# Performance work log

Measured on AMD Instinct MI355X. Metric: run time of the kernel, lower is better.

Reference implementation:

```python
import jax, jax.numpy as jnp
import numpy as np

N_SYS = 512      # number of crystal systems in the batch
N_ATOM = 32      # atoms per system (uniform for the reference)
N = N_SYS * N_ATOM            # 16384 total atoms
M = N_SYS * N_ATOM * N_ATOM   # 524288 dense intra-system edges
R = 16           # lattice translation points per edge
E = 128          # embed_dim
H = 8            # num_heads


def setup_inputs() -> dict:
    key = jax.random.key(0)
    ks = jax.random.split(key, 6)
    x = jax.random.normal(ks[0], (N, E), jnp.float32)
    in_proj_weight = jax.random.normal(ks[1], (3 * E, E), jnp.float32) / np.float32(np.sqrt(E))
    in_proj_bias = jnp.zeros((3 * E,), jnp.float32)
    out_proj_weight = jax.random.normal(ks[2], (E, E), jnp.float32) / np.float32(np.sqrt(E))
    out_proj_bias = jnp.zeros((E,), jnp.float32)
    # per-node per-head Gaussian exponents; must be negative for convergent lattice sums
    alpha = -(jax.random.uniform(ks[3], (N, H), jnp.float32) * 0.9 + 0.1)
    # squared distances from atom i to lattice images of atom j, up to ~5 Angstrom
    dist2 = jax.random.uniform(ks[4], (M, R), jnp.float32) * 25.0
    # dense intra-system edge list in (query-major) block order, as Crystalformer assumes
    base = (np.arange(N_SYS, dtype=np.int32) * N_ATOM)[:, None, None]
    qi = np.arange(N_ATOM, dtype=np.int32)[None, :, None]
    kj = np.arange(N_ATOM, dtype=np.int32)[None, None, :]
    e0 = np.broadcast_to(base + qi, (N_SYS, N_ATOM, N_ATOM)).reshape(-1)
    e1 = np.broadcast_to(base + kj, (N_SYS, N_ATOM, N_ATOM)).reshape(-1)
    edges = jnp.asarray(np.stack([e0, e1]), jnp.int32)
    batch = jnp.asarray(np.repeat(np.arange(N_SYS, dtype=np.int32), N_ATOM))
    return {
        "x": x,
        "in_proj_weight": in_proj_weight,
        "in_proj_bias": in_proj_bias,
        "out_proj_weight": out_proj_weight,
        "out_proj_bias": out_proj_bias,
        "alpha": alpha,
        "dist2": dist2,
        "edges": edges,
        "batch": batch,
    }


def reference(x, in_proj_weight, in_proj_bias, out_proj_weight, out_proj_bias,
              alpha, dist2, edges, batch):
    n, e = x.shape
    h = alpha.shape[1]
    dh = e // h
    # in-projection (self-attention: q = k = v = x)
    qkv = x @ in_proj_weight.T + in_proj_bias           # [N, 3E]
    q, k, v = jnp.split(qkv, 3, axis=-1)
    q = q.reshape(n, h, dh) / jnp.sqrt(jnp.asarray(dh, x.dtype))
    k = k.reshape(n, h, dh)
    v = v.reshape(n, h, dh)
    e0, e1 = edges[0], edges[1]
    # per-edge dot-product score, gathered q/k  -> [M, H]
    attn = jnp.einsum("mhd,mhd->mh", q[e0], k[e1])
    # real-domain lattice-sum attention bias: logsumexp_r(alpha_i * |r|^2)  -> [M, H]
    aw = jax.nn.logsumexp(alpha[e0][:, :, None] * dist2[:, None, :], axis=-1)
    s = attn + aw
    # segment softmax over each query's neighborhood (norm_func_mode=0 'default')
    smax = jax.ops.segment_max(s, e0, num_segments=n)   # [N, H]
    p = jnp.exp(s - smax[e0])
    denom = jax.ops.segment_sum(p, e0, num_segments=n)  # [N, H]
    p = p / denom[e0]
    # scatter-add aggregation of gathered values  -> [N, H, dh]
    out = jax.ops.segment_sum(p[:, :, None] * v[e1], e0, num_segments=n)
    # out-projection
    out = out.reshape(n, e) @ out_proj_weight.T + out_proj_bias
    return out
```

## Files before the change

### kernel.cpp

```cpp
#include <hip/hip_runtime.h>
#include <hip/hip_bf16.h>

#define LOG2E_F 1.4426950408889634f

typedef __attribute__((ext_vector_type(8))) short short8;
typedef __attribute__((ext_vector_type(4))) float f32x4;

__device__ inline unsigned short f2b(float f) {
    __hip_bfloat16 h = __float2bfloat16(f);
    return *reinterpret_cast<unsigned short*>(&h);
}

__device__ inline short8 load_frag_f32(const float* p) {
    const float4 lo = *(const float4*)p;
    const float4 hi = *(const float4*)(p + 4);
    short8 r;
    r[0] = (short)f2b(lo.x); r[1] = (short)f2b(lo.y);
    r[2] = (short)f2b(lo.z); r[3] = (short)f2b(lo.w);
    r[4] = (short)f2b(hi.x); r[5] = (short)f2b(hi.y);
    r[6] = (short)f2b(hi.z); r[7] = (short)f2b(hi.w);
    return r;
}

__global__ __launch_bounds__(512, 4) void fused_attn_kernel(
    const float* __restrict__ x, const float* __restrict__ Win,
    const float* __restrict__ bin, const float* __restrict__ Wout,
    const float* __restrict__ bout, const float* __restrict__ alpha,
    const float* __restrict__ dist2, float* __restrict__ out)
{
    __shared__ float qkvl[3][32][164];
    __shared__ unsigned short aggb[32][136];

    const int sys  = blockIdx.x;
    const int tid  = threadIdx.x;
    const int lane = tid & 63;
    const int wv   = tid >> 6;
    const int r16  = lane & 15;
    const int kg   = lane >> 4;
    const int base = sys << 5;

    short8 af[2][4];
    #pragma unroll
    for (int rt = 0; rt < 2; ++rt)
        #pragma unroll
        for (int ks = 0; ks < 4; ++ks)
            af[rt][ks] = load_frag_f32(
                x + (size_t)(base + rt * 16 + r16) * 128 + ks * 32 + kg * 8);

    #pragma unroll
    for (int j = 0; j < 3; ++j) {
        const int ct = wv * 3 + j;
        const int c  = ct * 16 + r16;
        short8 bf[4];
        #pragma unroll
        for (int ks = 0; ks < 4; ++ks)
            bf[ks] = load_frag_f32(Win + (size_t)c * 128 + ks * 32 + kg * 8);
        const float bias_v = bin[c];
        const int   bufi   = ct >> 3;
        const int   hh     = ct & 7;
        const float scale  = (bufi == 0) ? 0.25f : 1.0f;

        #pragma unroll
        for (int rt = 0; rt < 2; ++rt) {
            f32x4 acc = {0.f, 0.f, 0.f, 0.f};
            #pragma unroll
            for (int ks = 0; ks < 4; ++ks)
                acc = __builtin_amdgcn_mfma_f32_16x16x32_bf16(af[rt][ks], bf[ks], acc, 0, 0, 0);
            #pragma unroll
            for (int r = 0; r < 4; ++r) {
                const int atom = rt * 16 + kg * 4 + r;
                qkvl[bufi][atom][hh * 20 + r16] = (acc[r] + bias_v) * scale;
            }
        }
    }

    const int t     = tid & 255;
    const int khalf = tid >> 8;
    const int qi    = t >> 3;
    const int h     = t & 7;
    const float al2 = alpha[(size_t)(base + qi) * 8 + h] * LOG2E_F;

    __syncthreads();

    float qreg[16];
    {
        const float* qrow = &qkvl[0][qi][h * 20];
        #pragma unroll
        for (int d4 = 0; d4 < 4; ++d4) {
            const float4 tq = *(const float4*)(qrow + (d4 << 2));
            qreg[d4 * 4 + 0] = tq.x; qreg[d4 * 4 + 1] = tq.y;
            qreg[d4 * 4 + 2] = tq.z; qreg[d4 * 4 + 3] = tq.w;
        }
    }

    float m = -1e30f;
    float den = 0.f;
    float acc[16] = {};
    const float* dp = dist2 + ((size_t)(sys * 1024 + qi * 32) + khalf * 16) * 16;

    #pragma unroll
    for (int kk = 0; kk < 16; ++kk, dp += 16) {
        const int kj = khalf * 16 + kk;
        const float4 t0 = *(const float4*)(dp + 0);
        const float4 t1 = *(const float4*)(dp + 4);
        const float4 t2 = *(const float4*)(dp + 8);
        const float4 t3 = *(const float4*)(dp + 12);
        const float mn = fminf(
            fminf(fminf(fminf(t0.x, t0.y), fminf(t0.z, t0.w)),
                  fminf(fminf(t1.x, t1.y), fminf(t1.z, t1.w))),
            fminf(fminf(fminf(t2.x, t2.y), fminf(t2.z, t2.w)),
                  fminf(fminf(t3.x, t3.y), fminf(t3.z, t3.w))));
        const float c0 = al2 * mn;
        float e0 = __builtin_amdgcn_exp2f(fmaf(al2, t0.x, -c0));
        e0 += __builtin_amdgcn_exp2f(fmaf(al2, t0.y, -c0));
        e0 += __builtin_amdgcn_exp2f(fmaf(al2, t0.z, -c0));
        e0 += __builtin_amdgcn_exp2f(fmaf(al2, t0.w, -c0));
        float e1 = __builtin_amdgcn_exp2f(fmaf(al2, t1.x, -c0));
        e1 += __builtin_amdgcn_exp2f(fmaf(al2, t1.y, -c0));
        e1 += __builtin_amdgcn_exp2f(fmaf(al2, t1.z, -c0));
        e1 += __builtin_amdgcn_exp2f(fmaf(al2, t1.w, -c0));
        float e2 = __builtin_amdgcn_exp2f(fmaf(al2, t2.x, -c0));
        e2 += __builtin_amdgcn_exp2f(fmaf(al2, t2.y, -c0));
        e2 += __builtin_amdgcn_exp2f(fmaf(al2, t2.z, -c0));
        e2 += __builtin_amdgcn_exp2f(fmaf(al2, t2.w, -c0));
        float e3 = __builtin_amdgcn_exp2f(fmaf(al2, t3.x, -c0));
        e3 += __builtin_amdgcn_exp2f(fmaf(al2, t3.y, -c0));
        e3 += __builtin_amdgcn_exp2f(fmaf(al2, t3.z, -c0));
        e3 += __builtin_amdgcn_exp2f(fmaf(al2, t3.w, -c0));
        const float ssum = (e0 + e1) + (e2 + e3);

        const float* kr = &qkvl[1][kj][h * 20];
        const float4 k0 = *(const float4*)(kr + 0);
        const float4 k1 = *(const float4*)(kr + 4);
        const float4 k2 = *(const float4*)(kr + 8);
        const float4 k3 = *(const float4*)(kr + 12);
        float p0 = qreg[0] * k0.x, p1 = qreg[1] * k0.y;
        float p2 = qreg[2] * k0.z, p3 = qreg[3] * k0.w;
        p0 = fmaf(qreg[4],  k1.x, p0); p1 = fmaf(qreg[5],  k1.y, p1);
        p2 = fmaf(qreg[6],  k1.z, p2); p3 = fmaf(qreg[7],  k1.w, p3);
        p0 = fmaf(qreg[8],  k2.x, p0); p1 = fmaf(qreg[9],  k2.y, p1);
        p2 = fmaf(qreg[10], k2.z, p2); p3 = fmaf(qreg[11], k2.w, p3);
        p0 = fmaf(qreg[12], k3.x, p0); p1 = fmaf(qreg[13], k3.y, p1);
        p2 = fmaf(qreg[14], k3.z, p2); p3 = fmaf(qreg[15], k3.w, p3);
        const float dot = (p0 + p1) + (p2 + p3);

        const float b = fmaf(dot, LOG2E_F, c0);

        if (b - m > 8.0f) {
            const float sc = __builtin_amdgcn_exp2f(m - b);
            den *= sc;
            #pragma unroll
            for (int d = 0; d < 16; ++d) acc[d] *= sc;
            m = b;
        }
        const float p = __builtin_amdgcn_exp2f(b - m) * ssum;
        den += p;

        const float* vr = &qkvl[2][kj][h * 20];
        const float4 v0 = *(const float4*)(vr + 0);
        const float4 v1 = *(const float4*)(vr + 4);
        const float4 v2 = *(const float4*)(vr + 8);
        const float4 v3 = *(const float4*)(vr + 12);
        acc[0]  = fmaf(p, v0.x, acc[0]);  acc[1]  = fmaf(p, v0.y, acc[1]);
        acc[2]  = fmaf(p, v0.z, acc[2]);  acc[3]  = fmaf(p, v0.w, acc[3]);
        acc[4]  = fmaf(p, v1.x, acc[4]);  acc[5]  = fmaf(p, v1.y, acc[5]);
        acc[6]  = fmaf(p, v1.z, acc[6]);  acc[7]  = fmaf(p, v1.w, acc[7]);
        acc[8]  = fmaf(p, v2.x, acc[8]);  acc[9]  = fmaf(p, v2.y, acc[9]);
        acc[10] = fmaf(p, v2.z, acc[10]); acc[11] = fmaf(p, v2.w, acc[11]);
        acc[12] = fmaf(p, v3.x, acc[12]); acc[13] = fmaf(p, v3.y, acc[13]);
        acc[14] = fmaf(p, v3.z, acc[14]); acc[15] = fmaf(p, v3.w, acc[15]);
    }

    __syncthreads();
    float* exch = &qkvl[0][0][0];
    if (khalf == 1) {
        float* e = exch + t * 19;
        e[0] = m; e[1] = den;
        #pragma unroll
        for (int d = 0; d < 16; ++d) e[2 + d] = acc[d];
    }
    __syncthreads();
    if (khalf == 0) {
        const float* e = exch + t * 19;
        const float m2   = e[0];
        const float den2 = e[1];
        const float M  = fmaxf(m, m2);
        const float s1 = __builtin_amdgcn_exp2f(m - M);
        const float s2 = __builtin_amdgcn_exp2f(m2 - M);
        const float inv = 1.0f / (den * s1 + den2 * s2);
        const float a1 = s1 * inv, a2 = s2 * inv;

        unsigned short* op = &aggb[qi][h * 16];
        uint4 o0, o1;
        o0.x = (unsigned)f2b(fmaf(acc[0],  a1, e[2]  * a2)) | ((unsigned)f2b(fmaf(acc[1],  a1, e[3]  * a2)) << 16);
        o0.y = (unsigned)f2b(fmaf(acc[2],  a1, e[4]  * a2)) | ((unsigned)f2b(fmaf(acc[3],  a1, e[5]  * a2)) << 16);
        o0.z = (unsigned)f2b(fmaf(acc[4],  a1, e[6]  * a2)) | ((unsigned)f2b(fmaf(acc[5],  a1, e[7]  * a2)) << 16);
        o0.w = (unsigned)f2b(fmaf(acc[6],  a1, e[8]  * a2)) | ((unsigned)f2b(fmaf(acc[7],  a1, e[9]  * a2)) << 16);
        o1.x = (unsigned)f2b(fmaf(acc[8],  a1, e[10] * a2)) | ((unsigned)f2b(fmaf(acc[9],  a1, e[11] * a2)) << 16);
        o1.y = (unsigned)f2b(fmaf(acc[10], a1, e[12] * a2)) | ((unsigned)f2b(fmaf(acc[11], a1, e[13] * a2)) << 16);
        o1.z = (unsigned)f2b(fmaf(acc[12], a1, e[14] * a2)) | ((unsigned)f2b(fmaf(acc[13], a1, e[15] * a2)) << 16);
        o1.w = (unsigned)f2b(fmaf(acc[14], a1, e[16] * a2)) | ((unsigned)f2b(fmaf(acc[15], a1, e[17] * a2)) << 16);
        *(uint4*)op       = o0;
        *(uint4*)(op + 8) = o1;
    }

    __syncthreads();

    short8 aA[2][4];
    #pragma unroll
    for (int rt = 0; rt < 2; ++rt)
        #pragma unroll
        for (int ks = 0; ks < 4; ++ks)
            aA[rt][ks] = *(const short8*)(&aggb[rt * 16 + r16][ks * 32 + kg * 8]);

    {
        const int c = wv * 16 + r16;
        short8 bf[4];
        #pragma unroll
        for (int ks = 0; ks < 4; ++ks)
            bf[ks] = load_frag_f32(Wout + (size_t)c * 128 + ks * 32 + kg * 8);
        const float bias_v = bout[c];
        #pragma unroll
        for (int rt = 0; rt < 2; ++rt) {
            f32x4 oacc = {0.f, 0.f, 0.f, 0.f};
            #pragma unroll
            for (int ks = 0; ks < 4; ++ks)
                oacc = __builtin_amdgcn_mfma_f32_16x16x32_bf16(aA[rt][ks], bf[ks], oacc, 0, 0, 0);
            #pragma unroll
            for (int r = 0; r < 4; ++r) {
                const int row = base + rt * 16 + kg * 4 + r;
                out[(size_t)row * 128 + c] = oacc[r] + bias_v;
            }
        }
    }
}

extern "C" void kernel_launch(void* const* d_in, const int* in_sizes, int n_in,
                              void* d_out, int out_size, void* d_ws, size_t ws_size,
                              hipStream_t stream)
{
    const float* x     = (const float*)d_in[0];
    const float* Win   = (const float*)d_in[1];
    const float* bin   = (const float*)d_in[2];
    const float* Wout  = (const float*)d_in[3];
    const float* bout  = (const float*)d_in[4];
    const float* alpha = (const float*)d_in[5];
    const float* dist2 = (const float*)d_in[6];

    fused_attn_kernel<<<dim3(512), 512, 0, stream>>>(
        x, Win, bin, Wout, bout, alpha, dist2, (float*)d_out);
}
```

Baseline: 42.14 us.

## Split lattice-sum logsumexp bias into a separate precompute kernel

Adds a standalone kernel that computes log(sum_r exp2(alpha*log2e*dist2)) for every edge and head and writes it to workspace in head-major layout. The fused attention kernel then loads 16 precomputed bias values per thread instead of reading dist2 and evaluating the exponentials inline. The min-subtraction stabilisation of the exponent is dropped. The aim is to run the exponential-heavy work with more parallelism than the fused kernel allows. The cost is an extra launch and an extra 16 MB of intermediate traffic (written, then read back) on top of the existing 32 MB dist2 read.

After: 47.18 us. +12.0%, slower.

```diff
diff --git a/kernel.cpp b/kernel.cpp
--- a/kernel.cpp
+++ b/kernel.cpp
@@ -2,6 +2,7 @@
 #include <hip/hip_bf16.h>
 
 #define LOG2E_F 1.4426950408889634f
+#define M_EDGES 524288
 
 typedef __attribute__((ext_vector_type(8))) short short8;
 typedef __attribute__((ext_vector_type(4))) float f32x4;
@@ -22,11 +23,50 @@
     return r;
 }
 
+__global__ __launch_bounds__(256) void aw_kernel(
+    const float* __restrict__ alpha, const float* __restrict__ dist2,
+    float* __restrict__ aw2)
+{
+    const int m = blockIdx.x * 256 + threadIdx.x;
+    const float* dp = dist2 + (size_t)m * 16;
+    const float4 t0 = *(const float4*)(dp + 0);
+    const float4 t1 = *(const float4*)(dp + 4);
+    const float4 t2 = *(const float4*)(dp + 8);
+    const float4 t3 = *(const float4*)(dp + 12);
+
+    const float* ar = alpha + ((size_t)(m >> 5)) * 8;
+    const float4 a0 = *(const float4*)(ar);
+    const float4 a1 = *(const float4*)(ar + 4);
+    const float al[8] = {a0.x, a0.y, a0.z, a0.w, a1.x, a1.y, a1.z, a1.w};
+
+    #pragma unroll
+    for (int h = 0; h < 8; ++h) {
+        const float a = al[h] * LOG2E_F;
+        float e0 = __builtin_amdgcn_exp2f(a * t0.x);
+        e0 += __builtin_amdgcn_exp2f(a * t0.y);
+        e0 += __builtin_amdgcn_exp2f(a * t0.z);
+        e0 += __builtin_amdgcn_exp2f(a * t0.w);
+        float e1 = __builtin_amdgcn_exp2f(a * t1.x);
+        e1 += __builtin_amdgcn_exp2f(a * t1.y);
+        e1 += __builtin_amdgcn_exp2f(a * t1.z);
+        e1 += __builtin_amdgcn_exp2f(a * t1.w);
+        float e2 = __builtin_amdgcn_exp2f(a * t2.x);
+        e2 += __builtin_amdgcn_exp2f(a * t2.y);
+        e2 += __builtin_amdgcn_exp2f(a * t2.z);
+        e2 += __builtin_amdgcn_exp2f(a * t2.w);
+        float e3 = __builtin_amdgcn_exp2f(a * t3.x);
+        e3 += __builtin_amdgcn_exp2f(a * t3.y);
+        e3 += __builtin_amdgcn_exp2f(a * t3.z);
+        e3 += __builtin_amdgcn_exp2f(a * t3.w);
+        aw2[(size_t)h * M_EDGES + m] = __builtin_amdgcn_logf((e0 + e1) + (e2 + e3));
+    }
+}
+
 __global__ __launch_bounds__(512, 4) void fused_attn_kernel(
     const float* __restrict__ x, const float* __restrict__ Win,
     const float* __restrict__ bin, const float* __restrict__ Wout,
     const float* __restrict__ bout, const float* __restrict__ alpha,
-    const float* __restrict__ dist2, float* __restrict__ out)
+    const float* __restrict__ aw2, float* __restrict__ out)
 {
     __shared__ float qkvl[3][32][164];
     __shared__ unsigned short aggb[32][136];
@@ -78,7 +118,15 @@
     const int khalf = tid >> 8;
     const int qi    = t >> 3;
     const int h     = t & 7;
-    const float al2 = alpha[(size_t)(base + qi) * 8 + h] * LOG2E_F;
+
+    const float* awp = aw2 + (size_t)h * M_EDGES
+                     + (size_t)sys * 1024 + qi * 32 + khalf * 16;
+    const float4 w0 = *(const float4*)(awp + 0);
+    const float4 w1 = *(const float4*)(awp + 4);
+    const float4 w2 = *(const float4*)(awp + 8);
+    const float4 w3 = *(const float4*)(awp + 12);
+    const float awreg[16] = {w0.x, w0.y, w0.z, w0.w, w1.x, w1.y, w1.z, w1.w,
+                             w2.x, w2.y, w2.z, w2.w, w3.x, w3.y, w3.z, w3.w};
 
     __syncthreads();
 
@@ -96,39 +144,10 @@
     float m = -1e30f;
     float den = 0.f;
     float acc[16] = {};
-    const float* dp = dist2 + ((size_t)(sys * 1024 + qi * 32) + khalf * 16) * 16;
-
-    #pragma unroll
-    for (int kk = 0; kk < 16; ++kk, dp += 16) {
+
+    #pragma unroll
+    for (int kk = 0; kk < 16; ++kk) {
         const int kj = khalf * 16 + kk;
-        const float4 t0 = *(const float4*)(dp + 0);
-        const float4 t1 = *(const float4*)(dp + 4);
-        const float4 t2 = *(const float4*)(dp + 8);
-        const float4 t3 = *(const float4*)(dp + 12);
-        const float mn = fminf(
-            fminf(fminf(fminf(t0.x, t0.y), fminf(t0.z, t0.w)),
-                  fminf(fminf(t1.x, t1.y), fminf(t1.z, t1.w))),
-            fminf(fminf(fminf(t2.x, t2.y), fminf(t2.z, t2.w)),
-                  fminf(fminf(t3.x, t3.y), fminf(t3.z, t3.w))));
-        const float c0 = al2 * mn;
-        float e0 = __builtin_amdgcn_exp2f(fmaf(al2, t0.x, -c0));
-        e0 += __builtin_amdgcn_exp2f(fmaf(al2, t0.y, -c0));
-        e0 += __builtin_amdgcn_exp2f(fmaf(al2, t0.z, -c0));
-        e0 += __builtin_amdgcn_exp2f(fmaf(al2, t0.w, -c0));
-        float e1 = __builtin_amdgcn_exp2f(fmaf(al2, t1.x, -c0));
-        e1 += __builtin_amdgcn_exp2f(fmaf(al2, t1.y, -c0));
-        e1 += __builtin_amdgcn_exp2f(fmaf(al2, t1.z, -c0));
-        e1 += __builtin_amdgcn_exp2f(fmaf(al2, t1.w, -c0));
-        float e2 = __builtin_amdgcn_exp2f(fmaf(al2, t2.x, -c0));
-        e2 += __builtin_amdgcn_exp2f(fmaf(al2, t2.y, -c0));
-        e2 += __builtin_amdgcn_exp2f(fmaf(al2, t2.z, -c0));
-        e2 += __builtin_amdgcn_exp2f(fmaf(al2, t2.w, -c0));
-        float e3 = __builtin_amdgcn_exp2f(fmaf(al2, t3.x, -c0));
-        e3 += __builtin_amdgcn_exp2f(fmaf(al2, t3.y, -c0));
-        e3 += __builtin_amdgcn_exp2f(fmaf(al2, t3.z, -c0));
-        e3 += __builtin_amdgcn_exp2f(fmaf(al2, t3.w, -c0));
-        const float ssum = (e0 + e1) + (e2 + e3);
-
         const float* kr = &qkvl[1][kj][h * 20];
         const float4 k0 = *(const float4*)(kr + 0);
         const float4 k1 = *(const float4*)(kr + 4);
@@ -144,7 +163,7 @@
         p2 = fmaf(qreg[14], k3.z, p2); p3 = fmaf(qreg[15], k3.w, p3);
         const float dot = (p0 + p1) + (p2 + p3);
 
-        const float b = fmaf(dot, LOG2E_F, c0);
+        const float b = fmaf(dot, LOG2E_F, awreg[kk]);
 
         if (b - m > 8.0f) {
             const float sc = __builtin_amdgcn_exp2f(m - b);
@@ -153,7 +172,7 @@
             for (int d = 0; d < 16; ++d) acc[d] *= sc;
             m = b;
         }
-        const float p = __builtin_amdgcn_exp2f(b - m) * ssum;
+        const float p = __builtin_amdgcn_exp2f(b - m);
         den += p;
 
         const float* vr = &qkvl[2][kj][h * 20];
@@ -247,6 +266,9 @@
     const float* alpha = (const float*)d_in[5];
     const float* dist2 = (const float*)d_in[6];
 
+    float* aw2 = (float*)d_ws;
+
+    aw_kernel<<<dim3(2048), 256, 0, stream>>>(alpha, dist2, aw2);
     fused_attn_kernel<<<dim3(512), 512, 0, stream>>>(
-        x, Win, bin, Wout, bout, alpha, dist2, (float*)d_out);
-}
+        x, Win, bin, Wout, bout, alpha, aw2, (float*)d_out);
+}
```
